# Kernel tuning notes

Hardware: AMD Instinct MI355X
Metric: run time of the kernel (lower is better)

Reference implementation:

```python
import jax, jax.numpy as jnp
import numpy as np

NP, NA, E, DIN, DOUT = 50000, 50000, 800000, 128, 128


def setup_inputs() -> dict:
    key = jax.random.key(0)
    ks = jax.random.split(key, 16)
    inp = {
        'h_paper': jax.random.normal(ks[0], (NP, DIN), jnp.float32),
        'h_author': jax.random.normal(ks[1], (NA, DIN), jnp.float32),
        'W_r1': jax.random.normal(ks[2], (DIN, DOUT), jnp.float32) / np.sqrt(DIN),
        'W_r2': jax.random.normal(ks[3], (DIN, DOUT), jnp.float32) / np.sqrt(DIN),
        'W_r3': jax.random.normal(ks[4], (DIN, DOUT), jnp.float32) / np.sqrt(DIN),
        'att_W': jax.random.normal(ks[5], (DOUT, 128), jnp.float32) / np.sqrt(DOUT),
        'att_b': jax.random.normal(ks[6], (128,), jnp.float32) * 0.02,
        'att_q': jax.random.normal(ks[7], (128,), jnp.float32) / np.sqrt(128.0),
        'bn_gamma': jnp.ones((DOUT,), jnp.float32),
        'bn_beta': jnp.zeros((DOUT,), jnp.float32),
        'src_r1': jax.random.randint(ks[8], (E,), 0, NA, jnp.int32),
        'dst_r1': jax.random.randint(ks[9], (E,), 0, NP, jnp.int32),
        'src_r2': jax.random.randint(ks[10], (E,), 0, NP, jnp.int32),
        'dst_r2': jax.random.randint(ks[11], (E,), 0, NP, jnp.int32),
        'src_r3': jax.random.randint(ks[12], (E,), 0, NA, jnp.int32),
        'dst_r3': jax.random.randint(ks[13], (E,), 0, NA, jnp.int32),
    }
    return inp


def _graph_conv(h_src, W, src, dst, n_src, n_dst):
    # DGL GraphConv, norm='both', bias=False
    ones = jnp.ones(src.shape[0], h_src.dtype)
    deg_out = jnp.clip(jax.ops.segment_sum(ones, src, num_segments=n_src), 1.0)
    deg_in = jnp.clip(jax.ops.segment_sum(ones, dst, num_segments=n_dst), 1.0)
    m = (h_src * jax.lax.rsqrt(deg_out)[:, None]) @ W          # [n_src, Dout]
    agg = jax.ops.segment_sum(m[src], dst, num_segments=n_dst)  # [n_dst, Dout]
    return agg * jax.lax.rsqrt(deg_in)[:, None]


def _semantic_attention(z, att_W, att_b, att_q):
    # z: [R, N, D] per-relation outputs for one destination node type
    w = jnp.mean(jnp.tanh(z @ att_W + att_b) @ att_q, axis=1)  # [R]
    beta = jax.nn.softmax(w)
    return jnp.einsum('r,rnd->nd', beta, z)


def _post(x, gamma, beta):
    mu = jnp.mean(x, axis=0)
    var = jnp.var(x, axis=0)
    x = (x - mu) * jax.lax.rsqrt(var + 1e-5) * gamma + beta  # BatchNorm1d (train stats)
    return x * jax.lax.rsqrt(jnp.sum(x * x, axis=-1, keepdims=True) + 1e-12)  # L2 norm


def reference(h_paper, h_author, W_r1, W_r2, W_r3, att_W, att_b, att_q,
              bn_gamma, bn_beta, src_r1, dst_r1, src_r2, dst_r2, src_r3, dst_r3):
    n_p, n_a = h_paper.shape[0], h_author.shape[0]
    z_p1 = _graph_conv(h_author, W_r1, src_r1, dst_r1, n_a, n_p)  # author->paper
    z_p2 = _graph_conv(h_paper, W_r2, src_r2, dst_r2, n_p, n_p)   # paper->paper
    z_a1 = _graph_conv(h_author, W_r3, src_r3, dst_r3, n_a, n_a)  # author->author
    out_p = _semantic_attention(jnp.stack([z_p1, z_p2]), att_W, att_b, att_q)
    out_a = _semantic_attention(z_a1[None], att_W, att_b, att_q)
    out_p = _post(out_p, bn_gamma, bn_beta)
    out_a = _post(out_a, bn_gamma, bn_beta)
    return out_p, out_a
```

## Files before the change

### kernel.cpp

```cpp
#include <hip/hip_runtime.h>

#define DIM 128

static inline size_t align256(size_t x) { return (x + 255) & ~(size_t)255; }

__global__ void k_deg3(const int* __restrict__ s1, const int* __restrict__ d1, int E1,
                       const int* __restrict__ s2, const int* __restrict__ d2, int E2,
                       const int* __restrict__ s3, const int* __restrict__ d3, int E3,
                       int* __restrict__ dout, int* __restrict__ din, int NM) {
  int i = blockIdx.x * blockDim.x + threadIdx.x;
  int st = gridDim.x * blockDim.x;
  int ET = E1 + E2 + E3;
  for (; i < ET; i += st) {
    const int* sp; const int* dp; int j, r;
    if (i < E1) { r = 0; j = i; sp = s1; dp = d1; }
    else if (i < E1 + E2) { r = 1; j = i - E1; sp = s2; dp = d2; }
    else { r = 2; j = i - E1 - E2; sp = s3; dp = d3; }
    atomicAdd(&dout[r * NM + sp[j]], 1);
    atomicAdd(&din[r * NM + dp[j]], 1);
  }
}

__global__ __launch_bounds__(256) void k_scan1(const int* __restrict__ cnt,
                                               int* __restrict__ part, int M) {
  __shared__ int wsh[4];
  int t = threadIdx.x;
  int base = blockIdx.x * 2048 + t * 8;
  int s = 0;
  if (base + 8 <= M) {
    const int4* p = (const int4*)(cnt + base);
    int4 a = p[0], b = p[1];
    s = a.x + a.y + a.z + a.w + b.x + b.y + b.z + b.w;
  } else {
    for (int j = 0; j < 8; ++j) { int idx = base + j; if (idx < M) s += cnt[idx]; }
  }
#pragma unroll
  for (int off = 32; off; off >>= 1) s += __shfl_down(s, off, 64);
  int lane = t & 63, wid = t >> 6;
  if (lane == 0) wsh[wid] = s;
  __syncthreads();
  if (t == 0) part[blockIdx.x] = wsh[0] + wsh[1] + wsh[2] + wsh[3];
}

__global__ __launch_bounds__(256) void k_scan2(int* __restrict__ part, int B,
                                               int* __restrict__ rp, int M) {
  __shared__ int sh[256];
  int t = threadIdx.x;
  sh[t] = (t < B) ? part[t] : 0;
  __syncthreads();
  for (int off = 1; off < 256; off <<= 1) {
    int v = (t >= off) ? sh[t - off] : 0;
    __syncthreads();
    sh[t] += v;
    __syncthreads();
  }
  if (t < B) part[t] = t ? sh[t - 1] : 0;
  if (t == 0) rp[M] = sh[255];
}

__global__ __launch_bounds__(256) void k_scan3(const int* __restrict__ cnt,
                                               const int* __restrict__ part,
                                               int* __restrict__ rp,
                                               int* __restrict__ cur, int M) {
  __shared__ int wsh[4];
  int t = threadIdx.x, lane = t & 63, wid = t >> 6;
  int base = blockIdx.x * 2048 + t * 8;
  int v[8];
  if (base + 8 <= M) {
    const int4* p = (const int4*)(cnt + base);
    int4 a = p[0], b = p[1];
    v[0] = a.x; v[1] = a.y; v[2] = a.z; v[3] = a.w;
    v[4] = b.x; v[5] = b.y; v[6] = b.z; v[7] = b.w;
  } else {
    for (int j = 0; j < 8; ++j) { int idx = base + j; v[j] = (idx < M) ? cnt[idx] : 0; }
  }
  int ts = 0;
#pragma unroll
  for (int j = 0; j < 8; ++j) ts += v[j];
  int incl = ts;
#pragma unroll
  for (int d = 1; d < 64; d <<= 1) { int u = __shfl_up(incl, d, 64); if (lane >= d) incl += u; }
  if (lane == 63) wsh[wid] = incl;
  __syncthreads();
  int woff = 0;
  for (int w = 0; w < wid; ++w) woff += wsh[w];
  int run = part[blockIdx.x] + woff + incl - ts;
#pragma unroll
  for (int j = 0; j < 8; ++j) {
    int idx = base + j;
    if (idx < M) { rp[idx] = run; cur[idx] = run; }
    run += v[j];
  }
}

__global__ void k_fill3(const int* __restrict__ s1, const int* __restrict__ d1, int E1,
                        const int* __restrict__ s2, const int* __restrict__ d2, int E2,
                        const int* __restrict__ s3, const int* __restrict__ d3, int E3,
                        int* __restrict__ cur, int* __restrict__ col, int NM) {
  int i = blockIdx.x * blockDim.x + threadIdx.x;
  int st = gridDim.x * blockDim.x;
  int ET = E1 + E2 + E3;
  for (; i < ET; i += st) {
    const int* sp; const int* dp; int j, r;
    if (i < E1) { r = 0; j = i; sp = s1; dp = d1; }
    else if (i < E1 + E2) { r = 1; j = i - E1; sp = s2; dp = d2; }
    else { r = 2; j = i - E1 - E2; sp = s3; dp = d3; }
    int p = atomicAdd(&cur[r * NM + dp[j]], 1);
    col[p] = sp[j];
  }
}

__global__ __launch_bounds__(512) void k_gemm(const float* __restrict__ h,
                                              const float* __restrict__ W,
                                              const int* __restrict__ degout,
                                              float* __restrict__ m, int N) {
  __shared__ float Wl[DIM * DIM];
  for (int i = threadIdx.x; i < DIM * DIM; i += 512) Wl[i] = W[i];
  __syncthreads();
  int lane = threadIdx.x & 63, wid = threadIdx.x >> 6;
  int gw = blockIdx.x * 8 + wid, nw = gridDim.x * 8;
  for (int n = gw; n < N; n += nw) {
    float s = rsqrtf(fmaxf((float)degout[n], 1.0f));
    const float4* h4 = (const float4*)(h + (size_t)n * DIM);
    float ax = 0.f, ay = 0.f;
#pragma unroll 4
    for (int k4 = 0; k4 < 32; ++k4) {
      float4 hv = h4[k4];
      int k = k4 * 4;
      float2 w0 = *(const float2*)&Wl[(k + 0) * DIM + 2 * lane];
      float2 w1 = *(const float2*)&Wl[(k + 1) * DIM + 2 * lane];
      float2 w2 = *(const float2*)&Wl[(k + 2) * DIM + 2 * lane];
      float2 w3 = *(const float2*)&Wl[(k + 3) * DIM + 2 * lane];
      ax = fmaf(hv.x, w0.x, ax); ay = fmaf(hv.x, w0.y, ay);
      ax = fmaf(hv.y, w1.x, ax); ay = fmaf(hv.y, w1.y, ay);
      ax = fmaf(hv.z, w2.x, ax); ay = fmaf(hv.z, w2.y, ay);
      ax = fmaf(hv.w, w3.x, ax); ay = fmaf(hv.w, w3.y, ay);
    }
    float2 o; o.x = s * ax; o.y = s * ay;
    *(float2*)(m + (size_t)n * DIM + 2 * lane) = o;
  }
}

__global__ __launch_bounds__(256) void k_pull(const float* __restrict__ m,
                                              const int* __restrict__ rp,
                                              const int* __restrict__ col,
                                              float* __restrict__ z, int N) {
  int lane = threadIdx.x & 63, wid = threadIdx.x >> 6;
  int gw = blockIdx.x * 4 + wid, nw = gridDim.x * 4;
  for (int n = gw; n < N; n += nw) {
    int b = rp[n], e = rp[n + 1];
    float ax = 0.f, ay = 0.f;
    for (int idx = b; idx < e; ++idx) {
      int s = col[idx];
      float2 v = *(const float2*)(m + (size_t)s * DIM + 2 * lane);
      ax += v.x; ay += v.y;
    }
    float sc = rsqrtf(fmaxf((float)(e - b), 1.0f));
    float2 o; o.x = ax * sc; o.y = ay * sc;
    *(float2*)(z + (size_t)n * DIM + 2 * lane) = o;
  }
}

__global__ __launch_bounds__(512) void k_att(const float* __restrict__ z1,
                                             const float* __restrict__ z2,
                                             const float* __restrict__ attW,
                                             const float* __restrict__ attb,
                                             const float* __restrict__ attq,
                                             float* __restrict__ wsum, int N) {
  __shared__ float Wl[DIM * DIM];
  for (int i = threadIdx.x; i < DIM * DIM; i += 512) Wl[i] = attW[i];
  int lane = threadIdx.x & 63, wid = threadIdx.x >> 6;
  float b0 = attb[2 * lane], b1 = attb[2 * lane + 1];
  float q0 = attq[2 * lane], q1 = attq[2 * lane + 1];
  __syncthreads();
  int gw = blockIdx.x * 8 + wid, nw = gridDim.x * 8;
  float a1 = 0.f, a2 = 0.f;
  for (int n = gw; n < N; n += nw) {
    const float4* p1 = (const float4*)(z1 + (size_t)n * DIM);
    const float4* p2 = (const float4*)(z2 + (size_t)n * DIM);
    float c1x = 0, c1y = 0, c2x = 0, c2y = 0;
#pragma unroll 4
    for (int k4 = 0; k4 < 32; ++k4) {
      float4 u = p1[k4];
      float4 v = p2[k4];
      int k = k4 * 4;
      float2 w0 = *(const float2*)&Wl[(k + 0) * DIM + 2 * lane];
      float2 w1 = *(const float2*)&Wl[(k + 1) * DIM + 2 * lane];
      float2 w2 = *(const float2*)&Wl[(k + 2) * DIM + 2 * lane];
      float2 w3 = *(const float2*)&Wl[(k + 3) * DIM + 2 * lane];
      c1x = fmaf(u.x, w0.x, c1x); c1y = fmaf(u.x, w0.y, c1y);
      c2x = fmaf(v.x, w0.x, c2x); c2y = fmaf(v.x, w0.y, c2y);
      c1x = fmaf(u.y, w1.x, c1x); c1y = fmaf(u.y, w1.y, c1y);
      c2x = fmaf(v.y, w1.x, c2x); c2y = fmaf(v.y, w1.y, c2y);
      c1x = fmaf(u.z, w2.x, c1x); c1y = fmaf(u.z, w2.y, c1y);
      c2x = fmaf(v.z, w2.x, c2x); c2y = fmaf(v.z, w2.y, c2y);
      c1x = fmaf(u.w, w3.x, c1x); c1y = fmaf(u.w, w3.y, c1y);
      c2x = fmaf(v.w, w3.x, c2x); c2y = fmaf(v.w, w3.y, c2y);
    }
    a1 += tanhf(c1x + b0) * q0 + tanhf(c1y + b1) * q1;
    a2 += tanhf(c2x + b0) * q0 + tanhf(c2y + b1) * q1;
  }
#pragma unroll
  for (int off = 32; off; off >>= 1) {
    a1 += __shfl_down(a1, off, 64);
    a2 += __shfl_down(a2, off, 64);
  }
  __syncthreads();
  if (lane == 0) { Wl[wid] = a1; Wl[8 + wid] = a2; }
  __syncthreads();
  if (threadIdx.x == 0) {
    float s1 = 0, s2 = 0;
    for (int w = 0; w < 8; ++w) { s1 += Wl[w]; s2 += Wl[8 + w]; }
    atomicAdd(&wsum[0], s1);
    atomicAdd(&wsum[1], s2);
  }
}

__global__ void k_combine(float* __restrict__ x, const float* __restrict__ z2,
                          const float* __restrict__ wsum, float invN, int total4) {
  float w1 = wsum[0] * invN, w2 = wsum[1] * invN;
  float mx = fmaxf(w1, w2);
  float e1 = expf(w1 - mx), e2 = expf(w2 - mx);
  float inv = 1.f / (e1 + e2);
  float b1 = e1 * inv, b2 = e2 * inv;
  float4* x4 = (float4*)x;
  const float4* z4 = (const float4*)z2;
  int i = blockIdx.x * blockDim.x + threadIdx.x;
  int st = gridDim.x * blockDim.x;
  for (; i < total4; i += st) {
    float4 a = x4[i], b = z4[i];
    a.x = b1 * a.x + b2 * b.x;
    a.y = b1 * a.y + b2 * b.y;
    a.z = b1 * a.z + b2 * b.z;
    a.w = b1 * a.w + b2 * b.w;
    x4[i] = a;
  }
}

__global__ __launch_bounds__(128) void k_stats2(const float* __restrict__ xp,
                                                const float* __restrict__ xa,
                                                int NP, int NA, float* __restrict__ st) {
  int d = threadIdx.x;
  float sp = 0, qp = 0, sa = 0, qa = 0;
  for (int n = blockIdx.x; n < NP; n += gridDim.x) {
    float v = xp[(size_t)n * DIM + d]; sp += v; qp += v * v;
  }
  for (int n = blockIdx.x; n < NA; n += gridDim.x) {
    float v = xa[(size_t)n * DIM + d]; sa += v; qa += v * v;
  }
  atomicAdd(&st[d], sp);
  atomicAdd(&st[DIM + d], qp);
  atomicAdd(&st[2 * DIM + d], sa);
  atomicAdd(&st[3 * DIM + d], qa);
}

__global__ __launch_bounds__(256) void k_post2(float* __restrict__ xp, float* __restrict__ xa,
                                               const float* __restrict__ st,
                                               const float* __restrict__ gamma,
                                               const float* __restrict__ beta,
                                               int NP, int NA) {
  int lane = threadIdx.x & 63;
  int wv = blockIdx.x * 4 + (threadIdx.x >> 6), nw = gridDim.x * 4;
  int d0 = 2 * lane, d1 = d0 + 1;
  {
    float invN = 1.f / (float)NP;
    float mu0 = st[d0] * invN, mu1 = st[d1] * invN;
    float g0 = gamma[d0] * rsqrtf(st[DIM + d0] * invN - mu0 * mu0 + 1e-5f);
    float g1 = gamma[d1] * rsqrtf(st[DIM + d1] * invN - mu1 * mu1 + 1e-5f);
    float b0 = beta[d0], b1 = beta[d1];
    for (int n = wv; n < NP; n += nw) {
      float2 v = *(float2*)(xp + (size_t)n * DIM + d0);
      float y0 = fmaf(v.x - mu0, g0, b0);
      float y1 = fmaf(v.y - mu1, g1, b1);
      float p = y0 * y0 + y1 * y1;
#pragma unroll
      for (int off = 32; off; off >>= 1) p += __shfl_xor(p, off, 64);
      float r = rsqrtf(p + 1e-12f);
      float2 o; o.x = y0 * r; o.y = y1 * r;
      *(float2*)(xp + (size_t)n * DIM + d0) = o;
    }
  }
  {
    float invN = 1.f / (float)NA;
    float mu0 = st[2 * DIM + d0] * invN, mu1 = st[2 * DIM + d1] * invN;
    float g0 = gamma[d0] * rsqrtf(st[3 * DIM + d0] * invN - mu0 * mu0 + 1e-5f);
    float g1 = gamma[d1] * rsqrtf(st[3 * DIM + d1] * invN - mu1 * mu1 + 1e-5f);
    float b0 = beta[d0], b1 = beta[d1];
    for (int n = wv; n < NA; n += nw) {
      float2 v = *(float2*)(xa + (size_t)n * DIM + d0);
      float y0 = fmaf(v.x - mu0, g0, b0);
      float y1 = fmaf(v.y - mu1, g1, b1);
      float p = y0 * y0 + y1 * y1;
#pragma unroll
      for (int off = 32; off; off >>= 1) p += __shfl_xor(p, off, 64);
      float r = rsqrtf(p + 1e-12f);
      float2 o; o.x = y0 * r; o.y = y1 * r;
      *(float2*)(xa + (size_t)n * DIM + d0) = o;
    }
  }
}

extern "C" void kernel_launch(void* const* d_in, const int* in_sizes, int n_in,
                              void* d_out, int out_size, void* d_ws, size_t ws_size,
                              hipStream_t stream) {
  const float* h_paper  = (const float*)d_in[0];
  const float* h_author = (const float*)d_in[1];
  const float* W_r1 = (const float*)d_in[2];
  const float* W_r2 = (const float*)d_in[3];
  const float* W_r3 = (const float*)d_in[4];
  const float* att_W = (const float*)d_in[5];
  const float* att_b = (const float*)d_in[6];
  const float* att_q = (const float*)d_in[7];
  const float* bn_g = (const float*)d_in[8];
  const float* bn_b = (const float*)d_in[9];
  const int* src_r1 = (const int*)d_in[10];
  const int* dst_r1 = (const int*)d_in[11];
  const int* src_r2 = (const int*)d_in[12];
  const int* dst_r2 = (const int*)d_in[13];
  const int* src_r3 = (const int*)d_in[14];
  const int* dst_r3 = (const int*)d_in[15];

  int NP = in_sizes[0] / DIM;
  int NA = in_sizes[1] / DIM;
  int E1 = in_sizes[10], E2 = in_sizes[12], E3 = in_sizes[14];
  int NM = NP > NA ? NP : NA;
  int M = 3 * NM;
  int B = (M + 2047) / 2048;

  char* ws = (char*)d_ws;
  size_t off = 0;
  float* m_buf = (float*)(ws + off); off += align256((size_t)NM * DIM * 4);
  float* z2    = (float*)(ws + off); off += align256((size_t)NP * DIM * 4);
  int* col     = (int*)(ws + off);   off += align256(((size_t)E1 + E2 + E3) * 4);
  int* rp      = (int*)(ws + off);   off += align256(((size_t)M + 1) * 4);
  int* cur     = (int*)(ws + off);   off += align256((size_t)M * 4);
  int* part    = (int*)(ws + off);   off += align256(256 * 4);
  size_t zoff = off;
  int* din     = (int*)(ws + off);   off += (size_t)M * 4;
  int* dout    = (int*)(ws + off);   off += (size_t)M * 4;
  float* wsum  = (float*)(ws + off); off += 2 * 4;
  float* stats = (float*)(ws + off); off += 4 * DIM * 4;
  size_t zbytes = off - zoff;

  float* xp = (float*)d_out;
  float* xa = (float*)d_out + (size_t)NP * DIM;

  hipMemsetAsync(ws + zoff, 0, zbytes, stream);

  k_deg3<<<2048, 256, 0, stream>>>(src_r1, dst_r1, E1, src_r2, dst_r2, E2,
                                   src_r3, dst_r3, E3, dout, din, NM);

  k_scan1<<<B, 256, 0, stream>>>(din, part, M);
  k_scan2<<<1, 256, 0, stream>>>(part, B, rp, M);
  k_scan3<<<B, 256, 0, stream>>>(din, part, rp, cur, M);

  k_fill3<<<2048, 256, 0, stream>>>(src_r1, dst_r1, E1, src_r2, dst_r2, E2,
                                    src_r3, dst_r3, E3, cur, col, NM);

  k_gemm<<<512, 512, 0, stream>>>(h_author, W_r1, dout, m_buf, NA);
  k_pull<<<2048, 256, 0, stream>>>(m_buf, rp, col, xp, NP);
  k_gemm<<<512, 512, 0, stream>>>(h_paper, W_r2, dout + NM, m_buf, NP);
  k_pull<<<2048, 256, 0, stream>>>(m_buf, rp + NM, col, z2, NP);
  k_gemm<<<512, 512, 0, stream>>>(h_author, W_r3, dout + 2 * NM, m_buf, NA);
  k_pull<<<2048, 256, 0, stream>>>(m_buf, rp + 2 * NM, col, xa, NA);

  k_att<<<512, 512, 0, stream>>>(xp, z2, att_W, att_b, att_q, wsum, NP);
  k_combine<<<2048, 256, 0, stream>>>(xp, z2, wsum, 1.0f / (float)NP, NP * DIM / 4);

  k_stats2<<<1024, 128, 0, stream>>>(xp, xa, NP, NA, stats);
  k_post2<<<2048, 256, 0, stream>>>(xp, xa, stats, bn_g, bn_b, NP, NA);
}
```

Baseline: 1.109 ms.

## Replace per-node CSR with 64-node bucketed edge sort and LDS aggregation

Drops the per-destination in-degree CSR build (global atomics per edge) in favour of a two-pass block-local histogram and scatter into 64-node destination buckets, packing the local dst index and src id into one word. Aggregation now runs one block per bucket, summing gathered rows into a shared-memory accumulator with LDS atomics and counting in-degree there. This cuts global atomic contention during the sort, but adds LDS float atomics and only NB (~782) blocks of work per relation. The packing assumes source ids fit in 16 bits (50000 < 65536). Only 64 blocks handle the histogram and scatter.

```diff
diff --git a/kernel.cpp b/kernel.cpp
--- a/kernel.cpp
+++ b/kernel.cpp
@@ -1,24 +1,48 @@
 #include <hip/hip_runtime.h>
 
 #define DIM 128
+#define NBLK 64
+#define MAXTB 2560
 
 static inline size_t align256(size_t x) { return (x + 255) & ~(size_t)255; }
 
-__global__ void k_deg3(const int* __restrict__ s1, const int* __restrict__ d1, int E1,
-                       const int* __restrict__ s2, const int* __restrict__ d2, int E2,
-                       const int* __restrict__ s3, const int* __restrict__ d3, int E3,
-                       int* __restrict__ dout, int* __restrict__ din, int NM) {
+__global__ void k_dout(const int* __restrict__ s1, int E1,
+                       const int* __restrict__ s2, int E2,
+                       const int* __restrict__ s3, int E3,
+                       int* __restrict__ dout, int NM) {
   int i = blockIdx.x * blockDim.x + threadIdx.x;
   int st = gridDim.x * blockDim.x;
   int ET = E1 + E2 + E3;
   for (; i < ET; i += st) {
-    const int* sp; const int* dp; int j, r;
-    if (i < E1) { r = 0; j = i; sp = s1; dp = d1; }
-    else if (i < E1 + E2) { r = 1; j = i - E1; sp = s2; dp = d2; }
-    else { r = 2; j = i - E1 - E2; sp = s3; dp = d3; }
+    const int* sp; int j, r;
+    if (i < E1) { r = 0; j = i; sp = s1; }
+    else if (i < E1 + E2) { r = 1; j = i - E1; sp = s2; }
+    else { r = 2; j = i - E1 - E2; sp = s3; }
     atomicAdd(&dout[r * NM + sp[j]], 1);
-    atomicAdd(&din[r * NM + dp[j]], 1);
-  }
+  }
+}
+
+__global__ __launch_bounds__(256) void k_hist(const int* __restrict__ d1, int E1,
+                                              const int* __restrict__ d2, int E2,
+                                              const int* __restrict__ d3, int E3,
+                                              int* __restrict__ Hmat, int NB, int TB) {
+  __shared__ int hl[MAXTB];
+  int t = threadIdx.x, b = blockIdx.x;
+  for (int k = t; k < TB; k += 256) hl[k] = 0;
+  __syncthreads();
+  int ET = E1 + E2 + E3;
+  int CH = (ET + NBLK - 1) / NBLK;
+  int lo = b * CH, hi = min(lo + CH, ET);
+  for (int i = lo + t; i < hi; i += 256) {
+    const int* dp; int j, r;
+    if (i < E1) { r = 0; j = i; dp = d1; }
+    else if (i < E1 + E2) { r = 1; j = i - E1; dp = d2; }
+    else { r = 2; j = i - E1 - E2; dp = d3; }
+    int kb = r * NB + (dp[j] >> 6);
+    atomicAdd(&hl[kb], 1);
+  }
+  __syncthreads();
+  for (int k = t; k < TB; k += 256) Hmat[(size_t)k * NBLK + b] = hl[k];
 }
 
 __global__ __launch_bounds__(256) void k_scan1(const int* __restrict__ cnt,
@@ -93,20 +117,63 @@
   }
 }
 
-__global__ void k_fill3(const int* __restrict__ s1, const int* __restrict__ d1, int E1,
-                        const int* __restrict__ s2, const int* __restrict__ d2, int E2,
-                        const int* __restrict__ s3, const int* __restrict__ d3, int E3,
-                        int* __restrict__ cur, int* __restrict__ col, int NM) {
-  int i = blockIdx.x * blockDim.x + threadIdx.x;
-  int st = gridDim.x * blockDim.x;
+__global__ __launch_bounds__(256) void k_scatter(const int* __restrict__ s1, const int* __restrict__ d1, int E1,
+                                                 const int* __restrict__ s2, const int* __restrict__ d2, int E2,
+                                                 const int* __restrict__ s3, const int* __restrict__ d3, int E3,
+                                                 const int* __restrict__ rp,
+                                                 unsigned* __restrict__ ebuf, int NB, int TB) {
+  __shared__ int curl[MAXTB];
+  int t = threadIdx.x, b = blockIdx.x;
+  for (int k = t; k < TB; k += 256) curl[k] = rp[(size_t)k * NBLK + b];
+  __syncthreads();
   int ET = E1 + E2 + E3;
-  for (; i < ET; i += st) {
+  int CH = (ET + NBLK - 1) / NBLK;
+  int lo = b * CH, hi = min(lo + CH, ET);
+  for (int i = lo + t; i < hi; i += 256) {
     const int* sp; const int* dp; int j, r;
     if (i < E1) { r = 0; j = i; sp = s1; dp = d1; }
     else if (i < E1 + E2) { r = 1; j = i - E1; sp = s2; dp = d2; }
     else { r = 2; j = i - E1 - E2; sp = s3; dp = d3; }
-    int p = atomicAdd(&cur[r * NM + dp[j]], 1);
-    col[p] = sp[j];
+    int dst = dp[j];
+    int kb = r * NB + (dst >> 6);
+    int pos = atomicAdd(&curl[kb], 1);
+    ebuf[pos] = ((unsigned)(dst & 63) << 16) | (unsigned)sp[j];
+  }
+}
+
+__global__ __launch_bounds__(256) void k_agg(const float* __restrict__ m,
+                                             const unsigned* __restrict__ ebuf,
+                                             const int* __restrict__ rp,
+                                             int bucket0, float* __restrict__ z, int Ndst) {
+  __shared__ float acc[64][DIM];
+  __shared__ int dcnt[64];
+  int t = threadIdx.x, lane = t & 63, wid = t >> 6;
+  for (int i = t; i < 64 * DIM; i += 256) ((float*)acc)[i] = 0.f;
+  for (int i = t; i < 64; i += 256) dcnt[i] = 0;
+  __syncthreads();
+  int k = bucket0 + blockIdx.x;
+  int start = rp[(size_t)k * NBLK];
+  int end = rp[(size_t)(k + 1) * NBLK];
+  for (int e = start + wid; e < end; e += 4) {
+    unsigned p = ebuf[e];
+    int src = p & 0xFFFF;
+    int dl = p >> 16;
+    const float2 v = *(const float2*)(m + (size_t)src * DIM + 2 * lane);
+    atomicAdd(&acc[dl][2 * lane], v.x);
+    atomicAdd(&acc[dl][2 * lane + 1], v.y);
+    if (lane == 0) atomicAdd(&dcnt[dl], 1);
+  }
+  __syncthreads();
+  int base = blockIdx.x * 64;
+  for (int row = wid; row < 64; row += 4) {
+    int n = base + row;
+    if (n < Ndst) {
+      float sc = rsqrtf(fmaxf((float)dcnt[row], 1.0f));
+      float2 o;
+      o.x = acc[row][2 * lane] * sc;
+      o.y = acc[row][2 * lane + 1] * sc;
+      *(float2*)(z + (size_t)n * DIM + 2 * lane) = o;
+    }
   }
 }
 
@@ -138,26 +205,6 @@
     }
     float2 o; o.x = s * ax; o.y = s * ay;
     *(float2*)(m + (size_t)n * DIM + 2 * lane) = o;
-  }
-}
-
-__global__ __launch_bounds__(256) void k_pull(const float* __restrict__ m,
-                                              const int* __restrict__ rp,
-                                              const int* __restrict__ col,
-                                              float* __restrict__ z, int N) {
-  int lane = threadIdx.x & 63, wid = threadIdx.x >> 6;
-  int gw = blockIdx.x * 4 + wid, nw = gridDim.x * 4;
-  for (int n = gw; n < N; n += nw) {
-    int b = rp[n], e = rp[n + 1];
-    float ax = 0.f, ay = 0.f;
-    for (int idx = b; idx < e; ++idx) {
-      int s = col[idx];
-      float2 v = *(const float2*)(m + (size_t)s * DIM + 2 * lane);
-      ax += v.x; ay += v.y;
-    }
-    float sc = rsqrtf(fmaxf((float)(e - b), 1.0f));
-    float2 o; o.x = ax * sc; o.y = ay * sc;
-    *(float2*)(z + (size_t)n * DIM + 2 * lane) = o;
   }
 }
 
@@ -323,23 +370,26 @@
   int NP = in_sizes[0] / DIM;
   int NA = in_sizes[1] / DIM;
   int E1 = in_sizes[10], E2 = in_sizes[12], E3 = in_sizes[14];
+  int ET = E1 + E2 + E3;
   int NM = NP > NA ? NP : NA;
-  int M = 3 * NM;
+  int NB = (NM + 63) >> 6;
+  int TB = 3 * NB;
+  int M = TB * NBLK;
   int B = (M + 2047) / 2048;
 
   char* ws = (char*)d_ws;
   size_t off = 0;
-  float* m_buf = (float*)(ws + off); off += align256((size_t)NM * DIM * 4);
-  float* z2    = (float*)(ws + off); off += align256((size_t)NP * DIM * 4);
-  int* col     = (int*)(ws + off);   off += align256(((size_t)E1 + E2 + E3) * 4);
-  int* rp      = (int*)(ws + off);   off += align256(((size_t)M + 1) * 4);
-  int* cur     = (int*)(ws + off);   off += align256((size_t)M * 4);
-  int* part    = (int*)(ws + off);   off += align256(256 * 4);
+  float* m_buf = (float*)(ws + off);    off += align256((size_t)NM * DIM * 4);
+  float* z2    = (float*)(ws + off);    off += align256((size_t)NP * DIM * 4);
+  unsigned* ebuf = (unsigned*)(ws + off); off += align256((size_t)ET * 4);
+  int* Hmat    = (int*)(ws + off);      off += align256((size_t)M * 4);
+  int* rp      = (int*)(ws + off);      off += align256(((size_t)M + 1) * 4);
+  int* curscr  = (int*)(ws + off);      off += align256((size_t)M * 4);
+  int* part    = (int*)(ws + off);      off += align256(256 * 4);
   size_t zoff = off;
-  int* din     = (int*)(ws + off);   off += (size_t)M * 4;
-  int* dout    = (int*)(ws + off);   off += (size_t)M * 4;
-  float* wsum  = (float*)(ws + off); off += 2 * 4;
-  float* stats = (float*)(ws + off); off += 4 * DIM * 4;
+  int* dout    = (int*)(ws + off);      off += (size_t)3 * NM * 4;
+  float* wsum  = (float*)(ws + off);    off += 2 * 4;
+  float* stats = (float*)(ws + off);    off += 4 * DIM * 4;
   size_t zbytes = off - zoff;
 
   float* xp = (float*)d_out;
@@ -347,22 +397,21 @@
 
   hipMemsetAsync(ws + zoff, 0, zbytes, stream);
 
-  k_deg3<<<2048, 256, 0, stream>>>(src_r1, dst_r1, E1, src_r2, dst_r2, E2,
-                                   src_r3, dst_r3, E3, dout, din, NM);
-
-  k_scan1<<<B, 256, 0, stream>>>(din, part, M);
+  k_dout<<<2048, 256, 0, stream>>>(src_r1, E1, src_r2, E2, src_r3, E3, dout, NM);
+
+  k_hist<<<NBLK, 256, 0, stream>>>(dst_r1, E1, dst_r2, E2, dst_r3, E3, Hmat, NB, TB);
+  k_scan1<<<B, 256, 0, stream>>>(Hmat, part, M);
   k_scan2<<<1, 256, 0, stream>>>(part, B, rp, M);
-  k_scan3<<<B, 256, 0, stream>>>(din, part, rp, cur, M);
-
-  k_fill3<<<2048, 256, 0, stream>>>(src_r1, dst_r1, E1, src_r2, dst_r2, E2,
-                                    src_r3, dst_r3, E3, cur, col, NM);
+  k_scan3<<<B, 256, 0, stream>>>(Hmat, part, rp, curscr, M);
+  k_scatter<<<NBLK, 256, 0, stream>>>(src_r1, dst_r1, E1, src_r2, dst_r2, E2,
+                                      src_r3, dst_r3, E3, rp, ebuf, NB, TB);
 
   k_gemm<<<512, 512, 0, stream>>>(h_author, W_r1, dout, m_buf, NA);
-  k_pull<<<2048, 256, 0, stream>>>(m_buf, rp, col, xp, NP);
+  k_agg<<<NB, 256, 0, stream>>>(m_buf, ebuf, rp, 0, xp, NP);
   k_gemm<<<512, 512, 0, stream>>>(h_paper, W_r2, dout + NM, m_buf, NP);
-  k_pull<<<2048, 256, 0, stream>>>(m_buf, rp + NM, col, z2, NP);
+  k_agg<<<NB, 256, 0, stream>>>(m_buf, ebuf, rp, NB, z2, NP);
   k_gemm<<<512, 512, 0, stream>>>(h_author, W_r3, dout + 2 * NM, m_buf, NA);
-  k_pull<<<2048, 256, 0, stream>>>(m_buf, rp + 2 * NM, col, xa, NA);
+  k_agg<<<NB, 256, 0, stream>>>(m_buf, ebuf, rp, 2 * NB, xa, NA);
 
   k_att<<<512, 512, 0, stream>>>(xp, z2, att_W, att_b, att_q, wsum, NP);
   k_combine<<<2048, 256, 0, stream>>>(xp, z2, wsum, 1.0f / (float)NP, NP * DIM / 4);
```

Measured after the change: 2.798 ms. 152% more time.
